# Optimization experiments

Measured on AMD Instinct MI355X. Metric: run time of the kernel, lower is better.

## Reference

```python
import jax, jax.numpy as jnp
import numpy as np
import math

B, TQ, TK, D = 4, 1024, 1024, 1024
H, DK, DV = 16, 64, 64


def _ln(x, g, b, eps=1e-5):
    m = x.mean(-1, keepdims=True)
    v = ((x - m) ** 2).mean(-1, keepdims=True)
    return (x - m) * jax.lax.rsqrt(v + eps) * g + b


def setup_inputs() -> dict:
    key = jax.random.key(0)
    ks = jax.random.split(key, 24)
    s = 0.02
    inp = {
        "x": jax.random.normal(ks[0], (B, TQ, D), jnp.float32),
        "y": jax.random.normal(ks[1], (B, TK, D), jnp.float32),
        "mask": jax.random.randint(ks[2], (B, TK), 0, 2).astype(bool),
        # pre-attention layernorms (affine)
        "ln1_g": jnp.ones((D,)), "ln1_b": jnp.zeros((D,)),
        "ln2_g": jnp.ones((D,)), "ln2_b": jnp.zeros((D,)),
        # mha1 projections
        "q_w": jax.random.normal(ks[3], (D, H * DK)) * s, "q_b": jnp.zeros((H * DK,)),
        "k_w": jax.random.normal(ks[4], (D, H * DK)) * s, "k_b": jnp.zeros((H * DK,)),
        "v_w": jax.random.normal(ks[5], (D, H * DV)) * s, "v_b": jnp.zeros((H * DV,)),
        "o_w": jax.random.normal(ks[6], (H * DV, D)) * s, "o_b": jnp.zeros((D,)),
        # MLP: [LN, ReLU, Linear] x 2 over sizes [D, D, D]
        "mln1_g": jnp.ones((D,)), "mln1_b": jnp.zeros((D,)),
        "l1_w": jax.random.normal(ks[7], (D, D)) * s, "l1_b": jnp.zeros((D,)),
        "mln2_g": jnp.ones((D,)), "mln2_b": jnp.zeros((D,)),
        "l2_w": jax.random.normal(ks[8], (D, D)) * s, "l2_b": jnp.zeros((D,)),
    }
    return inp


def reference(x, y, mask, ln1_g, ln1_b, ln2_g, ln2_b,
              q_w, q_b, k_w, k_b, v_w, v_b, o_w, o_b,
              mln1_g, mln1_b, l1_w, l1_b, mln2_g, mln2_b, l2_w, l2_b):
    # pre-norm + relu
    x1 = jax.nn.relu(_ln(x, ln1_g, ln1_b))
    y1 = jax.nn.relu(_ln(y, ln2_g, ln2_b))
    # cross attention (mha1)
    b, t, _ = x1.shape
    q = (x1 @ q_w + q_b).reshape(b, t, H, DK)
    k = (y1 @ k_w + k_b).reshape(b, -1, H, DK)
    v = (y1 @ v_w + v_b).reshape(b, -1, H, DV)
    logits = jnp.einsum('bthd,bThd->bhtT', q, k) * (1.0 / math.sqrt(DK))
    logits = jnp.where(mask[:, None, None, :], logits, -1e30)
    w = jax.nn.softmax(logits, axis=-1)
    attn = jnp.einsum('bhtT,bThd->bthd', w, v).reshape(b, t, H * DV)
    x = x + (attn @ o_w + o_b)
    # MLP: LN -> ReLU -> Linear, twice
    h = jax.nn.relu(_ln(x, mln1_g, mln1_b)) @ l1_w + l1_b
    out = jax.nn.relu(_ln(h, mln2_g, mln2_b)) @ l2_w + l2_b
    return out
```

## Files before the change

### kernel.cpp

```cpp
#include <hip/hip_runtime.h>
#include <hip/hip_bf16.h>
#include <math.h>

#define D_MODEL 1024
#define NTOK    4096

typedef unsigned short u16;
typedef unsigned int   u32;
typedef __attribute__((ext_vector_type(8))) short  short8;
typedef __attribute__((ext_vector_type(4))) float  floatx4;
typedef __attribute__((ext_vector_type(4))) unsigned short ushort4v;
typedef __attribute__((ext_vector_type(2))) unsigned int   uint2v;

static __host__ __device__ __forceinline__ float bf2f(u16 u) {
    union { unsigned int i; float f; } v; v.i = ((unsigned int)u) << 16; return v.f;
}
static __host__ __device__ __forceinline__ u16 f2bf(float f) {
    union { float f; unsigned int i; } v; v.f = f;
    unsigned int r = (v.i + 0x7FFFu + ((v.i >> 16) & 1u)) >> 16;
    return (u16)r;
}
static __device__ __forceinline__ u32 fbits(float f) {
    union { float f; u32 i; } v; v.f = f; return v.i;
}
static __device__ __forceinline__ float fexp2(float x) {
    float r; asm("v_exp_f32 %0, %1" : "=v"(r) : "v"(x)); return r;
}
static __device__ __forceinline__ void gl2lds16(const void* g, void* l) {
    __builtin_amdgcn_global_load_lds(
        (const __attribute__((address_space(1))) void*)g,
        (__attribute__((address_space(3))) void*)l, 16, 0, 0);
}

__global__ __launch_bounds__(256) void CrossTransformer_27522150432886_kernel(
    float* __restrict__ out, int n, float val)
{
    int i = blockIdx.x * 256 + threadIdx.x;
    if (i < n) out[i] = val;
}

struct PreArgs {
    const float* w[6]; u16* wt;
    const float* x; const float* g1; const float* b1; u16* xn;
    const float* y; const float* g2; const float* b2; u16* yn;
    const void* maskp; float* madd;
};
__global__ __launch_bounds__(256) void pre_k(PreArgs a)
{
    __shared__ __align__(16) char shm[2176];
    const int blk = blockIdx.x, t = threadIdx.x;

    if (blk < 6144) {
        u16 (*tile)[33] = (u16(*)[33])shm;
        const int wz = blk >> 10, tl = blk & 1023;
        const int c0 = (tl & 31) * 32, r0 = (tl >> 5) * 32;
        const int tx = t & 31, ty = t >> 5;
        const float* W  = a.w[wz];
        u16*         Wt = a.wt + (size_t)wz * D_MODEL * D_MODEL;
#pragma unroll
        for (int j = 0; j < 4; j++)
            tile[ty + j * 8][tx] = f2bf(W[(size_t)(r0 + ty + j * 8) * D_MODEL + c0 + tx]);
        __syncthreads();
#pragma unroll
        for (int j = 0; j < 4; j++)
            Wt[(size_t)(c0 + ty + j * 8) * D_MODEL + r0 + tx] = tile[tx][ty + j * 8];
        return;
    }
    if (blk < 14336) {
        const int isY = blk >= 10240;
        const int row = blk - (isY ? 10240 : 6144);
        const float* in  = isY ? a.y  : a.x;
        const float* gam = isY ? a.g2 : a.g1;
        const float* bet = isY ? a.b2 : a.b1;
        u16*         out = isY ? a.yn : a.xn;
        float (*red)[4] = (float(*)[4])shm;

        const float4 p = *(const float4*)(in + (size_t)row * D_MODEL + t * 4);
        float v0 = p.x, v1 = p.y, v2 = p.z, v3 = p.w;
        float s = v0 + v1 + v2 + v3;
        float q = v0 * v0 + v1 * v1 + v2 * v2 + v3 * v3;
#pragma unroll
        for (int off = 32; off > 0; off >>= 1) {
            s += __shfl_xor(s, off, 64);
            q += __shfl_xor(q, off, 64);
        }
        if ((t & 63) == 0) { red[0][t >> 6] = s; red[1][t >> 6] = q; }
        __syncthreads();
        s = red[0][0] + red[0][1] + red[0][2] + red[0][3];
        q = red[1][0] + red[1][1] + red[1][2] + red[1][3];
        const float mean = s * (1.0f / D_MODEL);
        const float var  = q * (1.0f / D_MODEL) - mean * mean;
        const float rstd = rsqrtf(var + 1e-5f);
        const float4 gp = *(const float4*)(gam + t * 4);
        const float4 bp = *(const float4*)(bet + t * 4);
        ushort4v o;
        o[0] = f2bf(fmaxf((v0 - mean) * rstd * gp.x + bp.x, 0.f));
        o[1] = f2bf(fmaxf((v1 - mean) * rstd * gp.y + bp.y, 0.f));
        o[2] = f2bf(fmaxf((v2 - mean) * rstd * gp.z + bp.z, 0.f));
        o[3] = f2bf(fmaxf((v3 - mean) * rstd * gp.w + bp.w, 0.f));
        *(ushort4v*)(out + (size_t)row * D_MODEL + t * 4) = o;
        return;
    }
    {
        int* rb = (int*)shm;
        const unsigned int* wv = (const unsigned int*)a.maskp;
        int bad = 0;
        for (int i = t; i < 1024; i += 256) {
            unsigned int v = wv[i];
            if (!(v == 0u || v == 1u || v == 0xFFu || v == 0xFFFFFFFFu)) bad++;
        }
#pragma unroll
        for (int off = 32; off > 0; off >>= 1) bad += __shfl_xor(bad, off, 64);
        if ((t & 63) == 0) rb[t >> 6] = bad;
        __syncthreads();
        const int Bc = rb[0] + rb[1] + rb[2] + rb[3];
        if (Bc * 2 > 1024) {
            const unsigned char* b8 = (const unsigned char*)a.maskp;
            for (int i = t; i < 4096; i += 256) a.madd[i] = b8[i] ? 0.f : -1e30f;
        } else {
            const int* m32 = (const int*)a.maskp;
            for (int i = t; i < 4096; i += 256) a.madd[i] = m32[i] ? 0.f : -1e30f;
        }
    }
}

__global__ __launch_bounds__(256) void ln_relu_k(
    const void* __restrict__ in, const float* __restrict__ gam,
    const float* __restrict__ bet, u16* __restrict__ out)
{
    const int row = blockIdx.x, t = threadIdx.x;
    ushort4v u = *(const ushort4v*)((const u16*)in + (size_t)row * D_MODEL + t * 4);
    float v0 = bf2f(u[0]), v1 = bf2f(u[1]), v2 = bf2f(u[2]), v3 = bf2f(u[3]);
    float s = v0 + v1 + v2 + v3;
    float q = v0 * v0 + v1 * v1 + v2 * v2 + v3 * v3;
#pragma unroll
    for (int off = 32; off > 0; off >>= 1) {
        s += __shfl_xor(s, off, 64);
        q += __shfl_xor(q, off, 64);
    }
    __shared__ float red[2][4];
    if ((t & 63) == 0) { red[0][t >> 6] = s; red[1][t >> 6] = q; }
    __syncthreads();
    s = red[0][0] + red[0][1] + red[0][2] + red[0][3];
    q = red[1][0] + red[1][1] + red[1][2] + red[1][3];

    const float mean = s * (1.0f / D_MODEL);
    const float var  = q * (1.0f / D_MODEL) - mean * mean;
    const float rstd = rsqrtf(var + 1e-5f);

    const float4 gp = *(const float4*)(gam + t * 4);
    const float4 bp = *(const float4*)(bet + t * 4);
    ushort4v o;
    o[0] = f2bf(fmaxf((v0 - mean) * rstd * gp.x + bp.x, 0.f));
    o[1] = f2bf(fmaxf((v1 - mean) * rstd * gp.y + bp.y, 0.f));
    o[2] = f2bf(fmaxf((v2 - mean) * rstd * gp.z + bp.z, 0.f));
    o[3] = f2bf(fmaxf((v3 - mean) * rstd * gp.w + bp.w, 0.f));
    *(ushort4v*)(out + (size_t)row * D_MODEL + t * 4) = o;
}

struct GB {
    const u16* A; const u16* Bt; const float* bias; const float* resid;
    u16* C; float* Cf; float scale; int vt;
};
struct GB3 { GB g[3]; u16* VtG; };

__global__ __launch_bounds__(256) void gemm_qkv_k(GB3 gb)
{
    const int lin = blockIdx.x + 8 * blockIdx.y + 256 * blockIdx.z;
    const int t8  = (lin & 7) * 96 + (lin >> 3);
    const int z   = t8 >> 8;
    const int rem = t8 & 255;
    const GB cfg = gb.g[z];
    __shared__ __align__(16) u16 sm[3 * 8192];
    const int t = threadIdx.x, lane = t & 63, w = t >> 6;
    const int wy = w >> 1, wx = w & 1;
    const int bm = (rem >> 3) * 128, bn = (rem & 7) * 128;
    const int m = lane & 15, g = lane >> 4;
    const int arow = t >> 2;
    const int aseg = ((t & 3) ^ ((t >> 3) & 3)) * 8;
    const int gsw  = (g ^ ((m >> 1) & 3)) * 8;

    const u16* Ag = cfg.A  + (size_t)(bm + arow) * D_MODEL + aseg;
    const u16* Bg = cfg.Bt + (size_t)(bn + arow) * D_MODEL + aseg;

    auto stage = [&](int k0, int s) {
        char* dst = (char*)sm + s * 16384;
#pragma unroll
        for (int i = 0; i < 2; i++) {
            gl2lds16(Ag + (size_t)(i * 64) * D_MODEL + k0, dst + i * 4096 + w * 1024);
            gl2lds16(Bg + (size_t)(i * 64) * D_MODEL + k0, dst + 8192 + i * 4096 + w * 1024);
        }
    };

    floatx4 acc[4][4] = {};
    const int NT = D_MODEL / 32;

    stage(0, 0);
    stage(32, 1);
    asm volatile("s_waitcnt vmcnt(4)" ::: "memory");
    __builtin_amdgcn_s_barrier();

    int sb = 0;
    for (int tt = 0; tt < NT; ++tt) {
        int tp = tt + 2; if (tp >= NT) tp -= NT;
        int sbp = sb + 2; if (sbp >= 3) sbp -= 3;
        stage(tp * 32, sbp);

        const u16* As = sm + sb * 8192;
        const u16* Bs = As + 4096;
        short8 af[4], bf[4];
#pragma unroll
        for (int mt = 0; mt < 4; mt++)
            af[mt] = *(const short8*)(As + (wy * 64 + mt * 16 + m) * 32 + gsw);
#pragma unroll
        for (int nt = 0; nt < 4; nt++)
            bf[nt] = *(const short8*)(Bs + (wx * 64 + nt * 16 + m) * 32 + gsw);

        __builtin_amdgcn_s_setprio(1);
#pragma unroll
        for (int mt = 0; mt < 4; mt++)
#pragma unroll
            for (int nt = 0; nt < 4; nt++)
                acc[mt][nt] = __builtin_amdgcn_mfma_f32_16x16x32_bf16(
                    af[mt], bf[nt], acc[mt][nt], 0, 0, 0);
        __builtin_amdgcn_s_setprio(0);

        asm volatile("s_waitcnt vmcnt(4)" ::: "memory");
        __builtin_amdgcn_s_barrier();
        sb = sb + 1; if (sb >= 3) sb -= 3;
    }
    asm volatile("s_waitcnt vmcnt(0)" ::: "memory");
    __builtin_amdgcn_s_barrier();

    float bv[4];
#pragma unroll
    for (int nt = 0; nt < 4; nt++)
        bv[nt] = cfg.bias[bn + wx * 64 + nt * 16 + m];

    if (!cfg.vt) {
#pragma unroll
        for (int mt = 0; mt < 4; mt++)
#pragma unroll
            for (int r = 0; r < 4; r++) {
                const int grow = bm + wy * 64 + mt * 16 + g * 4 + r;
#pragma unroll
                for (int nt = 0; nt < 4; nt++) {
                    const int col = bn + wx * 64 + nt * 16 + m;
                    float val = (acc[mt][nt][r] + bv[nt]) * cfg.scale;
                    cfg.C[(size_t)grow * D_MODEL + col] = f2bf(val);
                }
            }
    } else {
        u16* Lt = sm;
        const int b16  = (bm >> 10) * 16;
        const int bn6  = bn >> 6;
        const int tok0 = bm & 1023;
#pragma unroll
        for (int hh = 0; hh < 2; hh++) {
            if (wx == hh) {
#pragma unroll
                for (int mt = 0; mt < 4; mt++)
#pragma unroll
                    for (int r = 0; r < 4; r++) {
                        const int tok = wy * 64 + mt * 16 + g * 4 + r;
#pragma unroll
                        for (int nt = 0; nt < 4; nt++) {
                            const int d = nt * 16 + m;
                            Lt[d * 128 + (((tok >> 3) ^ (d & 15)) << 3) + (tok & 7)] =
                                f2bf(acc[mt][nt][r] + bv[nt]);
                        }
                    }
            }
            __syncthreads();
#pragma unroll
            for (int j = 0; j < 4; j++) {
                const int s = j * 256 + t;
                const int d = s >> 4, c = s & 15;
                short8 v = *(const short8*)(Lt + d * 128 + ((c ^ (d & 15)) << 3));
                *(short8*)(gb.VtG + ((size_t)((b16 + bn6 + hh) * 64 + d)) * 1024 + tok0 + c * 8) = v;
            }
            __syncthreads();
        }
    }
}

__global__ __launch_bounds__(512) void gemm_out_k(GB cfg)
{
    const int lin = blockIdx.x + 8 * blockIdx.y;
    const int t8  = (lin & 7) * 32 + (lin >> 3);
    __shared__ __align__(16) u16 sm[3 * 8192];
    const int t = threadIdx.x, lane = t & 63, w = t >> 6;
    const int wy = w >> 2, wx = w & 3;
    const int bm = (t8 >> 3) * 128, bn = (t8 & 7) * 128;
    const int m = lane & 15, g = lane >> 4;
    const int arow = t >> 2;
    const int aseg = ((t & 3) ^ ((t >> 3) & 3)) * 8;
    const int gsw  = (g ^ ((m >> 1) & 3)) * 8;

    const u16* Ag = cfg.A  + (size_t)(bm + arow) * D_MODEL + aseg;
    const u16* Bg = cfg.Bt + (size_t)(bn + arow) * D_MODEL + aseg;

    auto stage = [&](int k0, int s) {
        char* dst = (char*)sm + s * 16384;
        gl2lds16(Ag + k0, dst + w * 1024);
        gl2lds16(Bg + k0, dst + 8192 + w * 1024);
    };

    floatx4 acc[4][2] = {};
    const int NT = D_MODEL / 32;

    stage(0, 0);
    stage(32, 1);
    asm volatile("s_waitcnt vmcnt(2)" ::: "memory");
    __builtin_amdgcn_s_barrier();

    int sb = 0;
    for (int tt = 0; tt < NT; ++tt) {
        int tp = tt + 2; if (tp >= NT) tp -= NT;
        int sbp = sb + 2; if (sbp >= 3) sbp -= 3;
        stage(tp * 32, sbp);

        const u16* As = sm + sb * 8192;
        const u16* Bs = As + 4096;
        short8 af[4], bf[2];
#pragma unroll
        for (int mt = 0; mt < 4; mt++)
            af[mt] = *(const short8*)(As + (wy * 64 + mt * 16 + m) * 32 + gsw);
#pragma unroll
        for (int nt = 0; nt < 2; nt++)
            bf[nt] = *(const short8*)(Bs + (wx * 32 + nt * 16 + m) * 32 + gsw);

        __builtin_amdgcn_s_setprio(1);
#pragma unroll
        for (int mt = 0; mt < 4; mt++)
#pragma unroll
            for (int nt = 0; nt < 2; nt++)
                acc[mt][nt] = __builtin_amdgcn_mfma_f32_16x16x32_bf16(
                    af[mt], bf[nt], acc[mt][nt], 0, 0, 0);
        __builtin_amdgcn_s_setprio(0);

        asm volatile("s_waitcnt vmcnt(2)" ::: "memory");
        __builtin_amdgcn_s_barrier();
        sb = sb + 1; if (sb >= 3) sb -= 3;
    }
    asm volatile("s_waitcnt vmcnt(0)" ::: "memory");

    float bv[2]; int cols[2];
#pragma unroll
    for (int nt = 0; nt < 2; nt++) {
        cols[nt] = bn + wx * 32 + nt * 16 + m;
        bv[nt]   = cfg.bias[cols[nt]];
    }
#pragma unroll
    for (int mt = 0; mt < 4; mt++) {
#pragma unroll
        for (int r = 0; r < 4; r++) {
            const int grow = bm + wy * 64 + mt * 16 + g * 4 + r;
#pragma unroll
            for (int nt = 0; nt < 2; nt++) {
                float val = acc[mt][nt][r] + bv[nt];
                if (cfg.resid) val += cfg.resid[(size_t)grow * D_MODEL + cols[nt]];
                if (cfg.Cf) cfg.Cf[(size_t)grow * D_MODEL + cols[nt]] = val;
                else        cfg.C [(size_t)grow * D_MODEL + cols[nt]] = f2bf(val);
            }
        }
    }
}

__global__ __launch_bounds__(256) void attn_k(
    const u16* __restrict__ Q, const u16* __restrict__ Kk,
    const u16* __restrict__ VtG, const float* __restrict__ maddG,
    u16* __restrict__ Ob)
{
    __shared__ __align__(16) char smraw[55808];
    u16*   KsB  = (u16*)smraw;
    u16*   VtB  = (u16*)(smraw + 16384);
    u16*   Ps   = (u16*)(smraw + 32768);
    float* madd = (float*)(smraw + 51200);
    float* liS  = (float*)(smraw + 55296);

    const int lin = blockIdx.x + 8 * (blockIdx.y + 16 * blockIdx.z);
    const int tw  = (lin & 7) * 64 + (lin >> 3);
    const int qt = tw & 7, h = (tw >> 3) & 15, b = tw >> 7;
    const int t = threadIdx.x, lane = t & 63, w = t >> 6;
    const int m = lane & 15, g = lane >> 4;

    for (int i = t; i < 1024; i += 256) madd[i] = maddG[b * 1024 + i];

    short8 qf[2][2];
    const u16* Qb = Q + ((size_t)(b * 1024 + qt * 128 + w * 32 + m)) * D_MODEL + h * 64 + g * 8;
#pragma unroll
    for (int q2 = 0; q2 < 2; q2++)
#pragma unroll
        for (int hf = 0; hf < 2; hf++)
            qf[q2][hf] = *(const short8*)(Qb + q2 * 16 * D_MODEL + hf * 32);

    u16* Pw = Ps + w * 32 * 72;
    const u16* Kp = Kk  + (size_t)(b * 1024) * D_MODEL + h * 64;
    const u16* Vp = VtG + (size_t)((b * 16 + h) * 64) * 1024;

    const int r0 = lane >> 3;
    const int ssl = ((lane & 7) ^ r0) * 8;
    auto stageKV = [&](int kt, int bufI) {
#pragma unroll
        for (int i = 0; i < 2; i++) {
            const int row = w * 16 + i * 8 + r0;
            gl2lds16(Kp + (size_t)(kt + row) * D_MODEL + ssl,
                     (char*)(KsB + bufI * 4096) + (w * 2 + i) * 1024);
            gl2lds16(Vp + (size_t)row * 1024 + kt + ssl,
                     (char*)(VtB + bufI * 4096) + (w * 2 + i) * 1024);
        }
    };

    floatx4 Ov[2][4] = {};
    float li[2] = { 0.f, 0.f };

    const int s8  = m & 7;
    const int sl0 = (g ^ s8) * 8;
    const int sl1 = sl0 ^ 32;

    stageKV(0, 0);
    __syncthreads();

    int buf = 0;
    for (int kt = 0; kt < 1024; kt += 64) {
        if (kt + 64 < 1024) stageKV(kt + 64, buf ^ 1);

        const u16* Ks = KsB + buf * 4096;
        const u16* Vt = VtB + buf * 4096;

        short8 af[4][2];
        float4 md[4];
#pragma unroll
        for (int tile = 0; tile < 4; tile++) {
            af[tile][0] = *(const short8*)(Ks + (tile * 16 + m) * 64 + sl0);
            af[tile][1] = *(const short8*)(Ks + (tile * 16 + m) * 64 + sl1);
            md[tile]    = *(const float4*)(madd + kt + tile * 16 + g * 4);
        }

#pragma unroll
        for (int q2 = 0; q2 < 2; q2++) {
            floatx4 st[4];
            __builtin_amdgcn_s_setprio(1);
#pragma unroll
            for (int tile = 0; tile < 4; tile++) {
                floatx4 z = {};
                z = __builtin_amdgcn_mfma_f32_16x16x32_bf16(af[tile][0], qf[q2][0], z, 0, 0, 0);
                st[tile] = __builtin_amdgcn_mfma_f32_16x16x32_bf16(af[tile][1], qf[q2][1], z, 0, 0, 0);
            }
            __builtin_amdgcn_s_setprio(0);
            float rs = 0.f;
#pragma unroll
            for (int tile = 0; tile < 4; tile++) {
                float p0 = fexp2(st[tile][0] + md[tile].x);
                float p1 = fexp2(st[tile][1] + md[tile].y);
                float p2 = fexp2(st[tile][2] + md[tile].z);
                float p3 = fexp2(st[tile][3] + md[tile].w);
                rs += (p0 + p1) + (p2 + p3);
                uint2v pk;
                pk[0] = __builtin_amdgcn_perm(fbits(p1), fbits(p0), 0x07060302u);
                pk[1] = __builtin_amdgcn_perm(fbits(p3), fbits(p2), 0x07060302u);
                *(uint2v*)(Pw + (q2 * 16 + m) * 72 + tile * 16 + g * 4) = pk;
            }
            rs += __shfl_xor(rs, 16, 64);
            rs += __shfl_xor(rs, 32, 64);
            li[q2] += rs;
        }

        short8 pa[2][2], vb[4][2];
#pragma unroll
        for (int q2 = 0; q2 < 2; q2++) {
            pa[q2][0] = *(const short8*)(Pw + (q2 * 16 + m) * 72 + g * 8);
            pa[q2][1] = *(const short8*)(Pw + (q2 * 16 + m) * 72 + 32 + g * 8);
        }
#pragma unroll
        for (int nt = 0; nt < 4; nt++) {
            vb[nt][0] = *(const short8*)(Vt + (nt * 16 + m) * 64 + sl0);
            vb[nt][1] = *(const short8*)(Vt + (nt * 16 + m) * 64 + sl1);
        }
        __builtin_amdgcn_s_setprio(1);
#pragma unroll
        for (int q2 = 0; q2 < 2; q2++)
#pragma unroll
            for (int nt = 0; nt < 4; nt++) {
                Ov[q2][nt] = __builtin_amdgcn_mfma_f32_16x16x32_bf16(
                    pa[q2][0], vb[nt][0], Ov[q2][nt], 0, 0, 0);
                Ov[q2][nt] = __builtin_amdgcn_mfma_f32_16x16x32_bf16(
                    pa[q2][1], vb[nt][1], Ov[q2][nt], 0, 0, 0);
            }
        __builtin_amdgcn_s_setprio(0);

        asm volatile("s_waitcnt vmcnt(0)" ::: "memory");
        __builtin_amdgcn_s_barrier();
        buf ^= 1;
    }

    if (g == 0) { liS[w * 32 + m] = li[0]; liS[w * 32 + 16 + m] = li[1]; }
    __builtin_amdgcn_s_waitcnt(0);
    float4 inv4[2];
#pragma unroll
    for (int q2 = 0; q2 < 2; q2++) {
        float4 l4 = *(const float4*)(liS + w * 32 + q2 * 16 + g * 4);
        inv4[q2].x = 1.0f / fmaxf(l4.x, 1e-37f);
        inv4[q2].y = 1.0f / fmaxf(l4.y, 1e-37f);
        inv4[q2].z = 1.0f / fmaxf(l4.z, 1e-37f);
        inv4[q2].w = 1.0f / fmaxf(l4.w, 1e-37f);
    }
#pragma unroll
    for (int q2 = 0; q2 < 2; q2++) {
        const float iv[4] = { inv4[q2].x, inv4[q2].y, inv4[q2].z, inv4[q2].w };
#pragma unroll
        for (int nt = 0; nt < 4; nt++)
#pragma unroll
            for (int r = 0; r < 4; r++) {
                const int tok = qt * 128 + w * 32 + q2 * 16 + g * 4 + r;
                Ob[(size_t)(b * 1024 + tok) * D_MODEL + h * 64 + nt * 16 + m] =
                    f2bf(Ov[q2][nt][r] * iv[r]);
            }
    }
}

extern "C" __attribute__((visibility("default")))
void kernel_launch(void* const* d_in, const int* in_sizes, int n_in,
                   void* d_out, int out_size, void* d_ws, size_t ws_size,
                   hipStream_t stream)
{
    (void)in_sizes; (void)n_in;
    const float* x      = (const float*)d_in[0];
    const float* y      = (const float*)d_in[1];
    const void*  maskp  = d_in[2];
    const float* ln1_g  = (const float*)d_in[3];
    const float* ln1_b  = (const float*)d_in[4];
    const float* ln2_g  = (const float*)d_in[5];
    const float* ln2_b  = (const float*)d_in[6];
    const float* q_w    = (const float*)d_in[7];
    const float* q_b    = (const float*)d_in[8];
    const float* k_w    = (const float*)d_in[9];
    const float* k_b    = (const float*)d_in[10];
    const float* v_w    = (const float*)d_in[11];
    const float* v_b    = (const float*)d_in[12];
    const float* o_w    = (const float*)d_in[13];
    const float* o_b    = (const float*)d_in[14];
    const float* mln1_g = (const float*)d_in[15];
    const float* mln1_b = (const float*)d_in[16];
    const float* l1_w   = (const float*)d_in[17];
    const float* l1_b   = (const float*)d_in[18];
    const float* mln2_g = (const float*)d_in[19];
    const float* mln2_b = (const float*)d_in[20];
    const float* l2_w   = (const float*)d_in[21];
    const float* l2_b   = (const float*)d_in[22];

    const int nout = out_size;
    const size_t MB = 1024 * 1024;
    if (ws_size < 61 * MB) {
        CrossTransformer_27522150432886_kernel<<<(nout + 255) / 256, 256, 0, stream>>>(
            (float*)d_out, nout, 7.0f);
        return;
    }

    char* ws = (char*)d_ws;
    const size_t WE = (size_t)D_MODEL * D_MODEL;
    u16*   wt   = (u16*)(ws);
    u16*   xn   = (u16*)(ws + 12 * MB);
    u16*   yn   = (u16*)(ws + 20 * MB);
    u16*   Qb   = (u16*)(ws + 28 * MB);
    u16*   Kb   = (u16*)(ws + 36 * MB);
    u16*   VtG  = (u16*)(ws + 44 * MB);
    u16*   attn = (u16*)(ws + 52 * MB);
    float* madd = (float*)(ws + 60 * MB);
    u16* x2 = xn; u16* m1n = Qb; u16* hb = Kb; u16* m2n = VtG;

    PreArgs pa;
    pa.w[0] = q_w; pa.w[1] = k_w; pa.w[2] = v_w;
    pa.w[3] = o_w; pa.w[4] = l1_w; pa.w[5] = l2_w;
    pa.wt = wt;
    pa.x = x; pa.g1 = ln1_g; pa.b1 = ln1_b; pa.xn = xn;
    pa.y = y; pa.g2 = ln2_g; pa.b2 = ln2_b; pa.yn = yn;
    pa.maskp = maskp; pa.madd = madd;
    pre_k<<<14337, 256, 0, stream>>>(pa);

    const float qscale = 0.18033688011112042f;
    GB3 qkv = {};
    qkv.g[0] = GB{ xn, wt + 0 * WE, q_b, nullptr, Qb, nullptr, qscale, 0 };
    qkv.g[1] = GB{ yn, wt + 1 * WE, k_b, nullptr, Kb, nullptr, 1.0f,  0 };
    qkv.g[2] = GB{ yn, wt + 2 * WE, v_b, nullptr, nullptr, nullptr, 1.0f, 1 };
    qkv.VtG = VtG;
    gemm_qkv_k<<<dim3(8, 32, 3), 256, 0, stream>>>(qkv);

    attn_k<<<dim3(8, 16, 4), 256, 0, stream>>>(Qb, Kb, VtG, madd, attn);

    GB go = GB{ attn, wt + 3 * WE, o_b, x, x2, nullptr, 1.0f, 0 };
    gemm_out_k<<<dim3(8, 32, 1), 512, 0, stream>>>(go);

    ln_relu_k<<<NTOK, 256, 0, stream>>>(x2, mln1_g, mln1_b, m1n);

    GB g1 = GB{ m1n, wt + 4 * WE, l1_b, nullptr, hb, nullptr, 1.0f, 0 };
    gemm_out_k<<<dim3(8, 32, 1), 512, 0, stream>>>(g1);

    ln_relu_k<<<NTOK, 256, 0, stream>>>(hb, mln2_g, mln2_b, m2n);

    GB g2 = GB{ m2n, wt + 5 * WE, l2_b, nullptr, nullptr, (float*)d_out, 1.0f, 0 };
    gemm_out_k<<<dim3(8, 32, 1), 512, 0, stream>>>(g2);
}
```

Measured before the change: 278.8 us.

## Enlarge QKV GEMM tiles to 256x256 with 512 threads and double-buffered LDS

Replaces the 128x128-tile QKV projection GEMM (768 blocks, 256 threads, triple-buffered 48KB LDS) with a 256x256-tile version using 512 threads, 128KB of dynamic shared memory and double-buffered 64-wide K steps. Larger tiles raise arithmetic intensity and cut global/L2 traffic per FLOP. The V transpose epilogue now writes 4-token vectors straight to global instead of staging through LDS. The cost is only 192 blocks, which is less than one wave on a 256-CU part, so some CUs sit idle. The scattered 8-byte transposed stores may also coalesce less well.

```diff
diff --git a/kernel.cpp b/kernel.cpp
--- a/kernel.cpp
+++ b/kernel.cpp
@@ -164,70 +164,69 @@
 };
 struct GB3 { GB g[3]; u16* VtG; };
 
-__global__ __launch_bounds__(256) void gemm_qkv_k(GB3 gb)
-{
-    const int lin = blockIdx.x + 8 * blockIdx.y + 256 * blockIdx.z;
-    const int t8  = (lin & 7) * 96 + (lin >> 3);
-    const int z   = t8 >> 8;
-    const int rem = t8 & 255;
+__global__ __launch_bounds__(512) void gemm_qkv256_k(GB3 gb)
+{
+    extern __shared__ char smc[];
+    const int lin = blockIdx.x;
+    const int t8  = (lin & 7) * 24 + (lin >> 3);
+    const int z   = t8 >> 6;
+    const int rem = t8 & 63;
     const GB cfg = gb.g[z];
-    __shared__ __align__(16) u16 sm[3 * 8192];
     const int t = threadIdx.x, lane = t & 63, w = t >> 6;
-    const int wy = w >> 1, wx = w & 1;
-    const int bm = (rem >> 3) * 128, bn = (rem & 7) * 128;
+    const int wy = w >> 2, wx = w & 3;
+    const int bm = (rem >> 2) * 256, bn = (rem & 3) * 256;
     const int m = lane & 15, g = lane >> 4;
-    const int arow = t >> 2;
-    const int aseg = ((t & 3) ^ ((t >> 3) & 3)) * 8;
-    const int gsw  = (g ^ ((m >> 1) & 3)) * 8;
-
-    const u16* Ag = cfg.A  + (size_t)(bm + arow) * D_MODEL + aseg;
-    const u16* Bg = cfg.Bt + (size_t)(bn + arow) * D_MODEL + aseg;
-
-    auto stage = [&](int k0, int s) {
-        char* dst = (char*)sm + s * 16384;
-#pragma unroll
-        for (int i = 0; i < 2; i++) {
-            gl2lds16(Ag + (size_t)(i * 64) * D_MODEL + k0, dst + i * 4096 + w * 1024);
-            gl2lds16(Bg + (size_t)(i * 64) * D_MODEL + k0, dst + 8192 + i * 4096 + w * 1024);
-        }
+    const int srcseg = ((t & 3) ^ ((t >> 3) & 3)) * 8;
+    const int gsw    = (g ^ ((m >> 1) & 3)) * 8;
+
+    const u16* Ag = cfg.A  + (size_t)(bm + (t >> 2)) * D_MODEL + srcseg;
+    const u16* Bg = cfg.Bt + (size_t)(bn + (t >> 2)) * D_MODEL + srcseg;
+
+    auto stage_half = [&](int kt, int s, int buf) {
+        const int koff = kt + s * 32;
+        char* base = smc + buf * 65536 + s * 32768;
+        gl2lds16(Ag + koff,                 base + t * 16);
+        gl2lds16(Ag + 128 * D_MODEL + koff, base + 8192 + t * 16);
+        gl2lds16(Bg + koff,                 base + 16384 + t * 16);
+        gl2lds16(Bg + 128 * D_MODEL + koff, base + 24576 + t * 16);
     };
 
-    floatx4 acc[4][4] = {};
-    const int NT = D_MODEL / 32;
-
-    stage(0, 0);
-    stage(32, 1);
-    asm volatile("s_waitcnt vmcnt(4)" ::: "memory");
-    __builtin_amdgcn_s_barrier();
-
-    int sb = 0;
+    floatx4 acc[8][4] = {};
+    const int NT = D_MODEL / 64;
+
+    stage_half(0, 0, 0);
+    stage_half(0, 1, 0);
+
+    int buf = 0;
     for (int tt = 0; tt < NT; ++tt) {
-        int tp = tt + 2; if (tp >= NT) tp -= NT;
-        int sbp = sb + 2; if (sbp >= 3) sbp -= 3;
-        stage(tp * 32, sbp);
-
-        const u16* As = sm + sb * 8192;
-        const u16* Bs = As + 4096;
-        short8 af[4], bf[4];
-#pragma unroll
-        for (int mt = 0; mt < 4; mt++)
-            af[mt] = *(const short8*)(As + (wy * 64 + mt * 16 + m) * 32 + gsw);
-#pragma unroll
-        for (int nt = 0; nt < 4; nt++)
-            bf[nt] = *(const short8*)(Bs + (wx * 64 + nt * 16 + m) * 32 + gsw);
-
-        __builtin_amdgcn_s_setprio(1);
-#pragma unroll
-        for (int mt = 0; mt < 4; mt++)
+        const int ktn = ((tt + 1) & (NT - 1)) * 64;
+        const int nbuf = buf ^ 1;
+#pragma unroll
+        for (int s = 0; s < 2; ++s) {
+            asm volatile("s_waitcnt vmcnt(4)" ::: "memory");
+            __builtin_amdgcn_s_barrier();
+            stage_half(ktn, s, nbuf);
+
+            const u16* As = (const u16*)(smc + buf * 65536 + s * 32768);
+            const u16* Bs = As + 8192;
+            short8 af[8], bf[4];
+#pragma unroll
+            for (int mt = 0; mt < 8; mt++)
+                af[mt] = *(const short8*)(As + (wy * 128 + mt * 16 + m) * 32 + gsw);
 #pragma unroll
             for (int nt = 0; nt < 4; nt++)
-                acc[mt][nt] = __builtin_amdgcn_mfma_f32_16x16x32_bf16(
-                    af[mt], bf[nt], acc[mt][nt], 0, 0, 0);
-        __builtin_amdgcn_s_setprio(0);
-
-        asm volatile("s_waitcnt vmcnt(4)" ::: "memory");
-        __builtin_amdgcn_s_barrier();
-        sb = sb + 1; if (sb >= 3) sb -= 3;
+                bf[nt] = *(const short8*)(Bs + (wx * 64 + nt * 16 + m) * 32 + gsw);
+
+            __builtin_amdgcn_s_setprio(1);
+#pragma unroll
+            for (int mt = 0; mt < 8; mt++)
+#pragma unroll
+                for (int nt = 0; nt < 4; nt++)
+                    acc[mt][nt] = __builtin_amdgcn_mfma_f32_16x16x32_bf16(
+                        af[mt], bf[nt], acc[mt][nt], 0, 0, 0);
+            __builtin_amdgcn_s_setprio(0);
+        }
+        buf ^= 1;
     }
     asm volatile("s_waitcnt vmcnt(0)" ::: "memory");
     __builtin_amdgcn_s_barrier();
@@ -239,10 +238,10 @@
 
     if (!cfg.vt) {
 #pragma unroll
-        for (int mt = 0; mt < 4; mt++)
+        for (int mt = 0; mt < 8; mt++)
 #pragma unroll
             for (int r = 0; r < 4; r++) {
-                const int grow = bm + wy * 64 + mt * 16 + g * 4 + r;
+                const int grow = bm + wy * 128 + mt * 16 + g * 4 + r;
 #pragma unroll
                 for (int nt = 0; nt < 4; nt++) {
                     const int col = bn + wx * 64 + nt * 16 + m;
@@ -251,35 +250,22 @@
                 }
             }
     } else {
-        u16* Lt = sm;
-        const int b16  = (bm >> 10) * 16;
-        const int bn6  = bn >> 6;
+        const int b    = bm >> 10;
         const int tok0 = bm & 1023;
 #pragma unroll
-        for (int hh = 0; hh < 2; hh++) {
-            if (wx == hh) {
-#pragma unroll
-                for (int mt = 0; mt < 4; mt++)
-#pragma unroll
-                    for (int r = 0; r < 4; r++) {
-                        const int tok = wy * 64 + mt * 16 + g * 4 + r;
-#pragma unroll
-                        for (int nt = 0; nt < 4; nt++) {
-                            const int d = nt * 16 + m;
-                            Lt[d * 128 + (((tok >> 3) ^ (d & 15)) << 3) + (tok & 7)] =
-                                f2bf(acc[mt][nt][r] + bv[nt]);
-                        }
-                    }
-            }
-            __syncthreads();
-#pragma unroll
-            for (int j = 0; j < 4; j++) {
-                const int s = j * 256 + t;
-                const int d = s >> 4, c = s & 15;
-                short8 v = *(const short8*)(Lt + d * 128 + ((c ^ (d & 15)) << 3));
-                *(short8*)(gb.VtG + ((size_t)((b16 + bn6 + hh) * 64 + d)) * 1024 + tok0 + c * 8) = v;
-            }
-            __syncthreads();
+        for (int mt = 0; mt < 8; mt++) {
+            const int tok = tok0 + wy * 128 + mt * 16 + g * 4;
+#pragma unroll
+            for (int nt = 0; nt < 4; nt++) {
+                const int col = bn + wx * 64 + nt * 16 + m;
+                const int h = col >> 6, d = col & 63;
+                ushort4v o;
+                o[0] = f2bf(acc[mt][nt][0] + bv[nt]);
+                o[1] = f2bf(acc[mt][nt][1] + bv[nt]);
+                o[2] = f2bf(acc[mt][nt][2] + bv[nt]);
+                o[3] = f2bf(acc[mt][nt][3] + bv[nt]);
+                *(ushort4v*)(gb.VtG + ((size_t)((b * 16 + h) * 64 + d)) * 1024 + tok) = o;
+            }
         }
     }
 }
@@ -558,6 +544,13 @@
         return;
     }
 
+    static bool attrSet = false;
+    if (!attrSet) {
+        hipFuncSetAttribute((const void*)gemm_qkv256_k,
+                            hipFuncAttributeMaxDynamicSharedMemorySize, 131072);
+        attrSet = true;
+    }
+
     char* ws = (char*)d_ws;
     const size_t WE = (size_t)D_MODEL * D_MODEL;
     u16*   wt   = (u16*)(ws);
@@ -585,7 +578,7 @@
     qkv.g[1] = GB{ yn, wt + 1 * WE, k_b, nullptr, Kb, nullptr, 1.0f,  0 };
     qkv.g[2] = GB{ yn, wt + 2 * WE, v_b, nullptr, nullptr, nullptr, 1.0f, 1 };
     qkv.VtG = VtG;
-    gemm_qkv_k<<<dim3(8, 32, 3), 256, 0, stream>>>(qkv);
+    gemm_qkv256_k<<<192, 512, 131072, stream>>>(qkv);
 
     attn_k<<<dim3(8, 16, 4), 256, 0, stream>>>(Qb, Kb, VtG, madd, attn);
 
```

Result: faster. 270.0 us (-3.2%).
